# Kernel tuning notes

Measured on AMD Instinct MI355X. Metric: run time of the kernel, lower is better.

The kernel has to match this reference:

```python
import jax, jax.numpy as jnp
import numpy as np

B, N, C, K = 4, 4096, 64, 32   # graphs, points/graph, feat dim, max_neighbors
R = 0.2                         # radius
H1, H2, H3 = 64, 64, 128        # edge-MLP widths (nn = MLP([C+3, 64, 64, 128]))


def setup_inputs() -> dict:
    key = jax.random.key(0)
    ks = jax.random.split(key, 6)
    x = jax.random.normal(ks[0], (B * N, C), jnp.float32)
    pos = jax.random.uniform(ks[1], (B * N, 3), jnp.float32)  # unit cube
    batch = jnp.repeat(jnp.arange(B, dtype=jnp.int32), N)      # sorted, equal-size graphs
    W1 = jax.random.normal(ks[2], (C + 3, H1), jnp.float32) * 0.1
    b1 = jnp.zeros((H1,), jnp.float32)
    W2 = jax.random.normal(ks[3], (H1, H2), jnp.float32) * 0.1
    b2 = jnp.zeros((H2,), jnp.float32)
    W3 = jax.random.normal(ks[4], (H2, H3), jnp.float32) * 0.1
    b3 = jnp.zeros((H3,), jnp.float32)
    return dict(x=x, pos=pos, batch=batch, W1=W1, b1=b1, W2=W2, b2=b2, W3=W3, b3=b3)


def reference(x, pos, batch, W1, b1, W2, b2, W3, b3):
    # ratio == 1.0 -> idx = all points (identity sampling per the torch code).
    posb = pos.reshape(B, N, 3)
    xb = x.reshape(B, N, C)

    # radius neighbor search within each graph: squared pairwise distances [B, N_tgt, N_src]
    p2 = jnp.sum(posb * posb, axis=-1)                              # [B,N]
    d2 = p2[:, :, None] + p2[:, None, :] - 2.0 * jnp.einsum('bnd,bmd->bnm', posb, posb)
    score = jnp.where(d2 <= R * R, -d2, -jnp.inf)                   # valid -> nearest-first
    top, nb = jax.lax.top_k(score, K)                               # [B,N,K] K nearest in ball
    valid = jnp.isfinite(top)                                        # self (d2=0) always valid -> covers add_self_loops

    gather = jax.vmap(lambda arr, idx: arr[idx])                     # per-graph gather
    x_j = gather(xb, nb)                                             # [B,N,K,C]
    pos_j = gather(posb, nb)                                         # [B,N,K,3]
    rel = pos_j - posb[:, :, None, :]                                # pos_j - pos_i

    # PointNetConv message: h = nn([x_j, pos_j - pos_i]); nn = Lin+ReLU x3
    h = jnp.concatenate([x_j, rel], axis=-1)                         # [B,N,K,C+3]
    h = jax.nn.relu(h @ W1 + b1)
    h = jax.nn.relu(h @ W2 + b2)
    h = jax.nn.relu(h @ W3 + b3)                                     # [B,N,K,H3]

    # max aggregation over neighbors (PointNetConv default aggr='max')
    neg = jnp.finfo(h.dtype).min
    h = jnp.where(valid[..., None], h, neg)
    out = jnp.max(h, axis=2).reshape(B * N, H3)                      # [B*N, 128]

    return out, pos, batch
```

## Files before the change

### kernel.cpp

```cpp
#include <hip/hip_runtime.h>
#include <hip/hip_bf16.h>
#include <float.h>
#include <stdint.h>

#define NPTS 4096
#define NB_K 32
#define CAP  256
#define CAPC 320

typedef short bf16x8 __attribute__((ext_vector_type(8)));
typedef float f32x4  __attribute__((ext_vector_type(4)));
#define MFMA_BF16 __builtin_amdgcn_mfma_f32_16x16x32_bf16
#define SCHED_FENCE() __builtin_amdgcn_sched_barrier(0)

__device__ __forceinline__ short bf16rne(float f) {
    unsigned u = __float_as_uint(f);
    unsigned r = u + 0x7fffu + ((u >> 16) & 1u);
    return (short)(r >> 16);
}
__device__ __forceinline__ short bfc(float f) {
    __hip_bfloat16 h = __float2bfloat16(f);
    return __builtin_bit_cast(short, h);
}

__global__ __launch_bounds__(256) void prep0_kernel(const float* __restrict__ W1,
                                                    const float* __restrict__ W2,
                                                    const float* __restrict__ W3,
                                                    short* __restrict__ frg,
                                                    unsigned* __restrict__ cnt) {
    const int tid = threadIdx.x;
    if (blockIdx.x == 9) {
        if (tid < 100) cnt[tid] = 0;
        return;
    }
    const int t = blockIdx.x * 256 + tid;
    const int frag = t >> 6, lane = t & 63;
    const int col16 = lane & 15, kg = lane >> 4;
    bf16x8 v;
    if (frag < 12) {
        const int s = frag >> 2, n = frag & 3;
        #pragma unroll
        for (int j = 0; j < 8; ++j) {
            const int k = s * 32 + kg * 8 + j;
            v[j] = (k < 67) ? bf16rne(W1[k * 64 + n * 16 + col16]) : (short)0;
        }
    } else if (frag < 20) {
        const int s = (frag - 12) >> 2, n = (frag - 12) & 3;
        #pragma unroll
        for (int j = 0; j < 8; ++j) {
            const int k = (2 * s + (j >> 2)) * 16 + kg * 4 + (j & 3);
            v[j] = bf16rne(W2[k * 64 + n * 16 + col16]);
        }
    } else {
        const int s = (frag - 20) >> 3, n = (frag - 20) & 7;
        #pragma unroll
        for (int j = 0; j < 8; ++j) {
            const int k = (2 * s + (j >> 2)) * 16 + kg * 4 + (j & 3);
            v[j] = bf16rne(W3[k * 128 + n * 16 + col16]);
        }
    }
    *(bf16x8*)(frg + (size_t)t * 8) = v;
}

__global__ __launch_bounds__(256) void bin_kernel(const float* __restrict__ pos,
                                                  float4* __restrict__ possrt,
                                                  unsigned* __restrict__ cnt) {
    __shared__ unsigned hist[25];
    __shared__ unsigned base[25];
    const int tid = threadIdx.x;
    const int id = blockIdx.x * 256 + tid;
    const int g = id >> 12;

    if (tid < 25) hist[tid] = 0;
    __syncthreads();

    const float px = pos[(size_t)id * 3 + 0];
    const float py = pos[(size_t)id * 3 + 1];
    const float pz = pos[(size_t)id * 3 + 2];
    int cx = (int)(px * 5.f); if (cx > 4) cx = 4;
    int cy = (int)(py * 5.f); if (cy > 4) cy = 4;
    const int c = cx * 5 + cy;
    const unsigned rank = atomicAdd(&hist[c], 1u);
    __syncthreads();

    if (tid < 25) base[tid] = atomicAdd(&cnt[g * 25 + tid], hist[tid]);
    __syncthreads();

    const unsigned slot = base[c] + rank;
    if (slot < CAPC) {
        float4 o;
        o.x = px; o.y = py; o.z = pz;
        o.w = __uint_as_float((unsigned)(id & (NPTS - 1)));
        possrt[(size_t)(g * 25 + c) * CAPC + slot] = o;
    }
}

__global__ __launch_bounds__(256, 4) void knn_kernel(const float* __restrict__ x,
                                                     const float* __restrict__ pos,
                                                     const float4* __restrict__ possrt,
                                                     const unsigned* __restrict__ cntArr,
                                                     unsigned short* __restrict__ nb16,
                                                     short* __restrict__ xb) {
    __shared__ int cand[8][CAP];
    __shared__ unsigned short nbl[4][32];
    const int tid = threadIdx.x;

    {
        const size_t base = ((size_t)blockIdx.x * 256 + tid) * 2;
        const float2 f = *(const float2*)(x + base);
        short2 o; o.x = bfc(f.x); o.y = bfc(f.y);
        *(short2*)(xb + base) = o;
    }

    const int wv = tid >> 6, lane = tid & 63;
    const int tgtA = (blockIdx.x * 4 + wv) * 2;
    const int g = tgtA >> 12;
    const unsigned long long ltm = (1ull << lane) - 1ull;
    const float RFILT = 0.040001f;
    const double RR = 0.2 * 0.2;
    const unsigned long long INF = ~0ull;

    for (int t = 0; t < 2; ++t) {
        const int tgt = tgtA + t;
        const float tx = pos[(size_t)tgt * 3 + 0];
        const float ty = pos[(size_t)tgt * 3 + 1];
        const float tz = pos[(size_t)tgt * 3 + 2];

        int cxl = (int)floorf((tx - 0.2001f) * 5.f); if (cxl < 0) cxl = 0;
        int cxh = (int)floorf((tx + 0.2001f) * 5.f); if (cxh > 4) cxh = 4;
        int cyl = (int)floorf((ty - 0.2001f) * 5.f); if (cyl < 0) cyl = 0;
        int cyh = (int)floorf((ty + 0.2001f) * 5.f); if (cyh > 4) cyh = 4;

        int* cd = cand[wv * 2 + t];
        int cnt = 0;
        for (int cx = cxl; cx <= cxh; ++cx)
            for (int cy = cyl; cy <= cyh; ++cy) {
                const int col = g * 25 + cx * 5 + cy;
                int n = (int)cntArr[col]; if (n > CAPC) n = CAPC;
                const int base = col * CAPC;
                for (int s0 = 0; s0 < n; s0 += 64) {
                    const int sl = s0 + lane;
                    bool want = false;
                    const int li = base + sl;
                    if (sl < n) {
                        const float4 cp = possrt[li];
                        const float dx = cp.x - tx, dy = cp.y - ty, dz = cp.z - tz;
                        const float d2 = fmaf(dx, dx, fmaf(dy, dy, dz * dz));
                        want = d2 <= RFILT;
                    }
                    const unsigned long long m = __ballot(want);
                    const int wp = cnt + __popcll(m & ltm);
                    if (want && wp < CAP) cd[wp] = li;
                    cnt += __popcll(m);
                }
            }
        if (cnt > CAP) cnt = CAP;

        const double txd = (double)tx, tyd = (double)ty, tzd = (double)tz;
        unsigned long long k0 = INF, k1 = INF, k2 = INF, k3 = INF;
#define LOADK(KS, S)                                                          \
        { const int p = lane + 64 * (S);                                      \
          if (p < cnt) {                                                      \
              const float4 cp = possrt[cd[p]];                                \
              const double ddx = (double)cp.x - txd;                          \
              const double ddy = (double)cp.y - tyd;                          \
              const double ddz = (double)cp.z - tzd;                          \
              const double dd = fma(ddx, ddx, fma(ddy, ddy, ddz * ddz));      \
              if (dd <= RR)                                                   \
                  KS = ((unsigned long long)__double_as_longlong(dd)          \
                        & ~0xfffULL)                                          \
                       | (unsigned long long)__float_as_uint(cp.w);           \
          } }
        LOADK(k0, 0) LOADK(k1, 1) LOADK(k2, 2) LOADK(k3, 3)
#undef LOADK

        const int cnt2 = __popcll(__ballot(k0 != INF)) + __popcll(__ballot(k1 != INF))
                       + __popcll(__ballot(k2 != INF)) + __popcll(__ballot(k3 != INF));

        unsigned long long pivot = 0xFFFFFFFFFFFFFFFEull;
        if (cnt2 > NB_K) {
            unsigned long long lo = 0, hi = 0x3FA5000000000000ull;
            for (int it = 0; it < 70; ++it) {
                const unsigned long long mid = lo + ((hi - lo) >> 1);
                const int c = __popcll(__ballot(k0 <= mid)) + __popcll(__ballot(k1 <= mid))
                            + __popcll(__ballot(k2 <= mid)) + __popcll(__ballot(k3 <= mid));
                if (c == NB_K) { pivot = mid; break; }
                if (c < NB_K) lo = mid + 1; else hi = mid - 1;
            }
        }

        int base = 0;
#define EMIT(KS)                                                              \
        { const bool sel = (KS <= pivot);                                     \
          const unsigned long long m = __ballot(sel);                         \
          const int wp = base + __popcll(m & ltm);                            \
          if (sel && wp < NB_K)                                               \
              nbl[wv][wp] = (unsigned short)(KS & 0xfff);                     \
          base += __popcll(m); }
        EMIT(k0) EMIT(k1) EMIT(k2) EMIT(k3)
#undef EMIT
        if (lane >= base && lane < NB_K)
            nbl[wv][lane] = (unsigned short)0xFFFF;

        unsigned v = (unsigned)nbl[wv][lane & 31];
        #pragma unroll
        for (int k = 2; k <= 32; k <<= 1)
            #pragma unroll
            for (int j = k >> 1; j > 0; j >>= 1) {
                const unsigned o = (unsigned)__shfl_xor((int)v, j);
                const bool lower = (lane & j) == 0;
                const bool up = (lane & k) == 0;
                const unsigned mn = v < o ? v : o;
                const unsigned mx = v < o ? o : v;
                v = (lower == up) ? mn : mx;
            }
        if (lane < NB_K)
            nb16[(size_t)tgt * NB_K + lane] = (unsigned short)v;
    }
}

__global__ __launch_bounds__(256, 4) void mlp_kernel(
    const short* __restrict__ xb, const float* __restrict__ pos, const int* __restrict__ batch,
    const float* __restrict__ b1, const float* __restrict__ b2, const float* __restrict__ b3,
    const unsigned short* __restrict__ nb16, const short* __restrict__ frg,
    float* __restrict__ out) {
    __shared__ short bfr[36 * 64 * 8];

    const int tid = threadIdx.x, wv = tid >> 6, lane = tid & 63;

    for (int i = tid; i < 36 * 64; i += 256)
        *(bf16x8*)(bfr + (size_t)i * 8) = *(const bf16x8*)(frg + (size_t)i * 8);
    __syncthreads();

    const int c0 = lane & 15, kg = lane >> 4, rlow = kg * 4;
    const int wbase = blockIdx.x * 4 + wv;
    const int gb = (wbase * 4) & ~(NPTS - 1);

    int nvAll[2];
    #pragma unroll
    for (int q = 0; q < 2; ++q)
        nvAll[q] = (int)nb16[(size_t)(wbase * 4 + q * 2 + (lane >> 5)) * 32 + (lane & 31)];

    for (int p = 0; p < 4; ++p) {
        const int tgt = wbase * 4 + p;
        const int nv = nvAll[p >> 1];
        const unsigned long long bm = __ballot(nv != 0xFFFF);
        const unsigned vmask = (p & 1) ? (unsigned)(bm >> 32) : (unsigned)bm;

        int jrow[2];
        #pragma unroll
        for (int mm = 0; mm < 2; ++mm) {
            const int j = __shfl(nv, (p & 1) * 32 + mm * 16 + c0);
            jrow[mm] = (j == 0xFFFF) ? 0 : j;
        }

        bf16x8 X1[2][3];
        #pragma unroll
        for (int mm = 0; mm < 2; ++mm) {
            const short* xr = xb + (size_t)(gb + jrow[mm]) * 64;
            #pragma unroll
            for (int s = 0; s < 2; ++s)
                X1[mm][s] = *(const bf16x8*)(xr + s * 32 + kg * 8);
            bf16x8 a = {0, 0, 0, 0, 0, 0, 0, 0};
            if (kg == 0) {
                const float* pj = pos + (size_t)(gb + jrow[mm]) * 3;
                const float* pi = pos + (size_t)tgt * 3;
                a[0] = bfc(pj[0] - pi[0]);
                a[1] = bfc(pj[1] - pi[1]);
                a[2] = bfc(pj[2] - pi[2]);
            }
            X1[mm][2] = a;
        }

        bf16x8 B2[2][2];
        #pragma unroll
        for (int nt = 0; nt < 4; ++nt) {
            const float4 bb = *(const float4*)(b1 + nt * 16 + rlow);
            f32x4 acc[2];
            acc[0] = acc[1] = f32x4{bb.x, bb.y, bb.z, bb.w};
            #pragma unroll
            for (int s = 0; s < 3; ++s) {
                const bf16x8 Wf = *(const bf16x8*)(bfr + (size_t)((s * 4 + nt) * 64 + lane) * 8);
                #pragma unroll
                for (int mm = 0; mm < 2; ++mm)
                    acc[mm] = MFMA_BF16(Wf, X1[mm][s], acc[mm], 0, 0, 0);
            }
            #pragma unroll
            for (int mm = 0; mm < 2; ++mm)
                #pragma unroll
                for (int r = 0; r < 4; ++r)
                    B2[mm][nt >> 1][(nt & 1) * 4 + r] = bfc(fmaxf(acc[mm][r], 0.f));
            SCHED_FENCE();
        }

        bf16x8 A3[2][2];
        #pragma unroll
        for (int nt = 0; nt < 4; ++nt) {
            const float4 bb = *(const float4*)(b2 + nt * 16 + rlow);
            f32x4 acc[2];
            acc[0] = acc[1] = f32x4{bb.x, bb.y, bb.z, bb.w};
            #pragma unroll
            for (int s = 0; s < 2; ++s) {
                const bf16x8 Wf = *(const bf16x8*)(bfr + (size_t)((12 + s * 4 + nt) * 64 + lane) * 8);
                #pragma unroll
                for (int mm = 0; mm < 2; ++mm)
                    acc[mm] = MFMA_BF16(Wf, B2[mm][s], acc[mm], 0, 0, 0);
            }
            #pragma unroll
            for (int mm = 0; mm < 2; ++mm)
                #pragma unroll
                for (int r = 0; r < 4; ++r)
                    A3[mm][nt >> 1][(nt & 1) * 4 + r] = bfc(fmaxf(acc[mm][r], 0.f));
            SCHED_FENCE();
        }

        #pragma unroll
        for (int n = 0; n < 8; ++n) {
            const float bv = b3[n * 16 + c0];
            f32x4 acc[2];
            acc[0] = acc[1] = f32x4{bv, bv, bv, bv};
            #pragma unroll
            for (int s = 0; s < 2; ++s) {
                const bf16x8 Bf = *(const bf16x8*)(bfr + (size_t)((20 + s * 8 + n) * 64 + lane) * 8);
                #pragma unroll
                for (int mm = 0; mm < 2; ++mm)
                    acc[mm] = MFMA_BF16(A3[mm][s], Bf, acc[mm], 0, 0, 0);
            }
            float v = 0.f;
            #pragma unroll
            for (int mm = 0; mm < 2; ++mm)
                #pragma unroll
                for (int r = 0; r < 4; ++r) {
                    const int row = mm * 16 + rlow + r;
                    const float h = fmaxf(acc[mm][r], 0.f);
                    v = fmaxf(v, ((vmask >> row) & 1u) ? h : 0.f);
                }
            v = fmaxf(v, __shfl_xor(v, 16));
            v = fmaxf(v, __shfl_xor(v, 32));
            if (lane < 16) out[(size_t)tgt * 128 + n * 16 + lane] = v;
            SCHED_FENCE();
        }

        if (lane < 3)  out[2097152 + (size_t)tgt * 3 + lane] = pos[(size_t)tgt * 3 + lane];
        if (lane == 3) out[2146304 + tgt] = (float)batch[tgt];
    }
}

extern "C" void kernel_launch(void* const* d_in, const int* in_sizes, int n_in,
                              void* d_out, int out_size, void* d_ws, size_t ws_size,
                              hipStream_t stream) {
    const float* x   = (const float*)d_in[0];
    const float* pos = (const float*)d_in[1];
    const int* batch = (const int*)d_in[2];
    const float* W1  = (const float*)d_in[3];
    const float* b1  = (const float*)d_in[4];
    const float* W2  = (const float*)d_in[5];
    const float* b2  = (const float*)d_in[6];
    const float* W3  = (const float*)d_in[7];
    const float* b3  = (const float*)d_in[8];
    float* out = (float*)d_out;

    char* ws = (char*)d_ws;
    short* xb            = (short*)ws;
    unsigned short* nb16 = (unsigned short*)(ws + (2 << 20));
    short* frg           = (short*)(ws + (3 << 20));
    unsigned* cnt        = (unsigned*)(ws + (3 << 20) + (64 << 10));
    float4* possrt       = (float4*)(ws + (3 << 20) + (128 << 10));

    hipLaunchKernelGGL(prep0_kernel, dim3(10), dim3(256), 0, stream, W1, W2, W3, frg, cnt);
    hipLaunchKernelGGL(bin_kernel, dim3(64), dim3(256), 0, stream, pos, possrt, cnt);
    hipLaunchKernelGGL(knn_kernel, dim3(2048), dim3(256), 0, stream,
                       x, pos, possrt, cnt, nb16, xb);
    hipLaunchKernelGGL(mlp_kernel, dim3(1024), dim3(256), 0, stream,
                       xb, pos, batch, b1, b2, b3, nb16, frg, out);
}
```

Baseline: 83.81 us.

## Group kNN targets by grid cell so each wave reuses candidate loads

The kNN kernel now gives each wave four target points taken from the same grid cell in the binned position array, instead of two consecutive target indices. It always scans the fixed 3x3 neighbourhood of that cell, and each candidate loaded from possrt is tested against all four targets before per-target ballot compaction. Output indices are recovered from the stored point id, which removes the per-target cell-range computation and the repeated candidate loads. The trade-offs are that some waves exit early when their cell has few points, register pressure rises, and a target is only processed if its binned slot fits within the cell capacity.

Result: slower. 88.87 us (+6.0%).

```diff
diff --git a/kernel.cpp b/kernel.cpp
--- a/kernel.cpp
+++ b/kernel.cpp
@@ -96,12 +96,11 @@
 }
 
 __global__ __launch_bounds__(256, 4) void knn_kernel(const float* __restrict__ x,
-                                                     const float* __restrict__ pos,
                                                      const float4* __restrict__ possrt,
                                                      const unsigned* __restrict__ cntArr,
                                                      unsigned short* __restrict__ nb16,
                                                      short* __restrict__ xb) {
-    __shared__ int cand[8][CAP];
+    __shared__ int cand[4][4][CAP];
     __shared__ unsigned short nbl[4][32];
     const int tid = threadIdx.x;
 
@@ -113,50 +112,67 @@
     }
 
     const int wv = tid >> 6, lane = tid & 63;
-    const int tgtA = (blockIdx.x * 4 + wv) * 2;
-    const int g = tgtA >> 12;
+    const int W = blockIdx.x * 4 + wv;
+    const int col = W % 100;
+    const int q = W / 100;
+    int n0 = (int)cntArr[col]; if (n0 > CAPC) n0 = CAPC;
+    if (q * 4 >= n0) return;
+
     const unsigned long long ltm = (1ull << lane) - 1ull;
     const float RFILT = 0.040001f;
     const double RR = 0.2 * 0.2;
     const unsigned long long INF = ~0ull;
 
-    for (int t = 0; t < 2; ++t) {
-        const int tgt = tgtA + t;
-        const float tx = pos[(size_t)tgt * 3 + 0];
-        const float ty = pos[(size_t)tgt * 3 + 1];
-        const float tz = pos[(size_t)tgt * 3 + 2];
-
-        int cxl = (int)floorf((tx - 0.2001f) * 5.f); if (cxl < 0) cxl = 0;
-        int cxh = (int)floorf((tx + 0.2001f) * 5.f); if (cxh > 4) cxh = 4;
-        int cyl = (int)floorf((ty - 0.2001f) * 5.f); if (cyl < 0) cyl = 0;
-        int cyh = (int)floorf((ty + 0.2001f) * 5.f); if (cyh > 4) cyh = 4;
-
-        int* cd = cand[wv * 2 + t];
-        int cnt = 0;
-        for (int cx = cxl; cx <= cxh; ++cx)
-            for (int cy = cyl; cy <= cyh; ++cy) {
-                const int col = g * 25 + cx * 5 + cy;
-                int n = (int)cntArr[col]; if (n > CAPC) n = CAPC;
-                const int base = col * CAPC;
-                for (int s0 = 0; s0 < n; s0 += 64) {
-                    const int sl = s0 + lane;
-                    bool want = false;
-                    const int li = base + sl;
-                    if (sl < n) {
-                        const float4 cp = possrt[li];
-                        const float dx = cp.x - tx, dy = cp.y - ty, dz = cp.z - tz;
+    const int g = col / 25, cell = col % 25, cx = cell / 5, cy = cell % 5;
+    const int cxl = cx > 0 ? cx - 1 : 0, cxh = cx < 4 ? cx + 1 : 4;
+    const int cyl = cy > 0 ? cy - 1 : 0, cyh = cy < 4 ? cy + 1 : 4;
+
+    float tx[4], ty[4], tz[4];
+    int tidx[4]; bool tval[4];
+    int tcnt[4] = {0, 0, 0, 0};
+    #pragma unroll
+    for (int t = 0; t < 4; ++t) {
+        const int slot = q * 4 + t;
+        tval[t] = slot < n0;
+        const float4 tp = possrt[(size_t)col * CAPC + (tval[t] ? slot : 0)];
+        tx[t] = tp.x; ty[t] = tp.y; tz[t] = tp.z;
+        tidx[t] = (int)__float_as_uint(tp.w);
+    }
+
+    for (int cx2 = cxl; cx2 <= cxh; ++cx2)
+        for (int cy2 = cyl; cy2 <= cyh; ++cy2) {
+            const int col2 = g * 25 + cx2 * 5 + cy2;
+            int n = (int)cntArr[col2]; if (n > CAPC) n = CAPC;
+            const int base = col2 * CAPC;
+            for (int s0 = 0; s0 < n; s0 += 64) {
+                const int sl = s0 + lane;
+                const int li = base + sl;
+                bool wt[4] = {false, false, false, false};
+                if (sl < n) {
+                    const float4 cp = possrt[li];
+                    #pragma unroll
+                    for (int t = 0; t < 4; ++t) {
+                        const float dx = cp.x - tx[t], dy = cp.y - ty[t], dz = cp.z - tz[t];
                         const float d2 = fmaf(dx, dx, fmaf(dy, dy, dz * dz));
-                        want = d2 <= RFILT;
+                        wt[t] = d2 <= RFILT;
                     }
-                    const unsigned long long m = __ballot(want);
-                    const int wp = cnt + __popcll(m & ltm);
-                    if (want && wp < CAP) cd[wp] = li;
-                    cnt += __popcll(m);
                 }
-            }
-        if (cnt > CAP) cnt = CAP;
-
-        const double txd = (double)tx, tyd = (double)ty, tzd = (double)tz;
+                #pragma unroll
+                for (int t = 0; t < 4; ++t) {
+                    const unsigned long long m = __ballot(wt[t]);
+                    const int wp = tcnt[t] + __popcll(m & ltm);
+                    if (wt[t] && wp < CAP) cand[wv][t][wp] = li;
+                    tcnt[t] += __popcll(m);
+                }
+            }
+        }
+
+    for (int t = 0; t < 4; ++t) {
+        if (!tval[t]) continue;
+        int cnt = tcnt[t]; if (cnt > CAP) cnt = CAP;
+        const int* cd = cand[wv][t];
+        const double txd = (double)tx[t], tyd = (double)ty[t], tzd = (double)tz[t];
+
         unsigned long long k0 = INF, k1 = INF, k2 = INF, k3 = INF;
 #define LOADK(KS, S)                                                          \
         { const int p = lane + 64 * (S);                                      \
@@ -214,8 +230,9 @@
                 const unsigned mx = v < o ? o : v;
                 v = (lower == up) ? mn : mx;
             }
+        const int gtgt = g * NPTS + tidx[t];
         if (lane < NB_K)
-            nb16[(size_t)tgt * NB_K + lane] = (unsigned short)v;
+            nb16[(size_t)gtgt * NB_K + lane] = (unsigned short)v;
     }
 }
 
@@ -370,7 +387,7 @@
     hipLaunchKernelGGL(prep0_kernel, dim3(10), dim3(256), 0, stream, W1, W2, W3, frg, cnt);
     hipLaunchKernelGGL(bin_kernel, dim3(64), dim3(256), 0, stream, pos, possrt, cnt);
     hipLaunchKernelGGL(knn_kernel, dim3(2048), dim3(256), 0, stream,
-                       x, pos, possrt, cnt, nb16, xb);
+                       x, possrt, cnt, nb16, xb);
     hipLaunchKernelGGL(mlp_kernel, dim3(1024), dim3(256), 0, stream,
                        xb, pos, batch, b1, b2, b3, nb16, frg, out);
 }
```
